# Kernel tuning notes

Measured on AMD Instinct MI355X. Metric: run time of the kernel, lower is better.

## Reference

```python
import jax, jax.numpy as jnp
import numpy as np

N_HEADS = 4
D_K = 64


def setup_inputs() -> dict:
    key = jax.random.key(0)
    k1, k2, k3, k4, k5 = jax.random.split(key, 5)
    C = 256
    return {
        "x": jax.random.normal(k1, (16, C, 32, 32), dtype=jnp.float32),
        "W_qkv": jax.random.normal(k2, (C, N_HEADS * D_K * 3), dtype=jnp.float32) * (C ** -0.5),
        "b_qkv": jax.random.normal(k3, (N_HEADS * D_K * 3,), dtype=jnp.float32) * 0.02,
        "W_out": jax.random.normal(k4, (N_HEADS * D_K, C), dtype=jnp.float32) * ((N_HEADS * D_K) ** -0.5),
        "b_out": jax.random.normal(k5, (C,), dtype=jnp.float32) * 0.02,
    }


def reference(x, W_qkv, b_qkv, W_out, b_out):
    # NOTE: the original forward never applies self.norm and ignores t.
    B, C, H, W = x.shape
    N = H * W
    scale = D_K ** -0.5
    xf = x.reshape(B, C, N).transpose(0, 2, 1)            # [B, N, C]
    qkv = (xf @ W_qkv + b_qkv).reshape(B, N, N_HEADS, 3 * D_K)
    q, k, v = jnp.split(qkv, 3, axis=-1)                  # each [B, N, H, dk]
    attn = jnp.einsum('bihd,bjhd->bijh', q, k) * scale    # [B, N, N, H]
    attn = jax.nn.softmax(attn, axis=2)                   # softmax over keys (j)
    res = jnp.einsum('bijh,bjhd->bihd', attn, v)          # [B, N, H, dk]
    res = res.reshape(B, N, N_HEADS * D_K)
    res = res @ W_out + b_out + xf                        # residual on flattened x
    return res.transpose(0, 2, 1).reshape(B, C, H, W)
```

## Files before the change

kernel.cpp:

```cpp
#include <hip/hip_runtime.h>
#include <math.h>

#define NN 1024

typedef __attribute__((ext_vector_type(8))) __bf16 bf16x8;
typedef __attribute__((ext_vector_type(4))) __bf16 bf16x4;
typedef __attribute__((ext_vector_type(4))) float f32x4;

__device__ __forceinline__ unsigned short f2bf(float f) {
    __bf16 h = (__bf16)f;
    return *(unsigned short*)&h;
}
__device__ __forceinline__ ushort4 pack4(float a, float b, float c, float d) {
    bf16x4 v;
    v[0] = (__bf16)a; v[1] = (__bf16)b; v[2] = (__bf16)c; v[3] = (__bf16)d;
    return *(ushort4*)&v;
}

__device__ __forceinline__ void async_cp16(const unsigned short* g, unsigned short* l) {
    __builtin_amdgcn_global_load_lds(
        (const __attribute__((address_space(1))) unsigned int*)g,
        (__attribute__((address_space(3))) unsigned int*)l,
        16, 0, 0);
}

__global__ __launch_bounds__(256) void prep_transpose(
    const float* __restrict__ x, const float* __restrict__ Wq,
    const float* __restrict__ Wo,
    unsigned short* __restrict__ xb, unsigned short* __restrict__ Wqt,
    unsigned short* __restrict__ Wot)
{
    __shared__ __align__(16) unsigned short T[64 * 72];
    const int bx = blockIdx.x;
    const int rt = blockIdx.y;
    const float* src; unsigned short* dst; int ncol, c0;
    if (bx < 256) {
        int b = bx >> 4; int ct = bx & 15;
        src = x + (size_t)b * 256 * 1024; dst = xb + (size_t)b * 1024 * 256;
        ncol = 1024; c0 = ct * 64;
    } else if (bx < 268) {
        src = Wq; dst = Wqt; ncol = 768; c0 = (bx - 256) * 64;
    } else {
        src = Wo; dst = Wot; ncol = 256; c0 = (bx - 268) * 64;
    }
    const int t = threadIdx.x;
    #pragma unroll
    for (int i = 0; i < 4; ++i) {
        int r  = i * 16 + (t >> 4);
        int c4 = (t & 15) * 4;
        float4 v = *(const float4*)&src[(size_t)(rt * 64 + r) * ncol + c0 + c4];
        *(ushort4*)&T[r * 72 + c4] = pack4(v.x, v.y, v.z, v.w);
    }
    __syncthreads();
    #pragma unroll
    for (int i = 0; i < 2; ++i) {
        int task = t + 256 * i;
        int c = task & 63, rs = task >> 6;
        ushort u8[8];
        #pragma unroll
        for (int k = 0; k < 8; ++k) u8[k] = T[(rs * 8 + k) * 72 + c];
        *(uint4*)&dst[(size_t)(c0 + c) * 256 + rt * 64 + rs * 8] = *(uint4*)u8;
    }
}

__global__ __launch_bounds__(256, 4) void qkv_gemm(
    const unsigned short* __restrict__ xb, const unsigned short* __restrict__ Wqt,
    const float* __restrict__ bias,
    unsigned short* __restrict__ Qb, unsigned short* __restrict__ Kb,
    unsigned short* __restrict__ Vtb)
{
    __shared__ __align__(16) unsigned short As[128 * 40];
    __shared__ __align__(16) unsigned short Bs[128 * 40];
    const int jt = blockIdx.x;
    const int m0 = blockIdx.y * 128;
    const int b  = m0 >> 10;
    const int n0 = m0 & 1023;
    const int t = threadIdx.x;
    const int w = t >> 6, lane = t & 63, quad = lane >> 4, cc = lane & 15;
    const int wm = (w & 1) * 64;
    const int wj = (w >> 1) * 64;

    f32x4 acc[4][4];
    #pragma unroll
    for (int ms = 0; ms < 4; ++ms)
        #pragma unroll
        for (int js = 0; js < 4; ++js) acc[ms][js] = (f32x4)(0.f);

    for (int k0 = 0; k0 < 256; k0 += 32) {
        __syncthreads();
        #pragma unroll
        for (int i = 0; i < 2; ++i) {
            int flat = t + 256 * i;
            int row = flat >> 2, seg = flat & 3;
            *(uint4*)&As[row * 40 + seg * 8] =
                *(const uint4*)&xb[(size_t)(m0 + row) * 256 + k0 + seg * 8];
            *(uint4*)&Bs[row * 40 + seg * 8] =
                *(const uint4*)&Wqt[(size_t)(jt * 128 + row) * 256 + k0 + seg * 8];
        }
        __syncthreads();
        bf16x8 af[4], bfr[4];
        #pragma unroll
        for (int ms = 0; ms < 4; ++ms)
            af[ms] = *(bf16x8*)&As[(wm + ms * 16 + cc) * 40 + quad * 8];
        #pragma unroll
        for (int js = 0; js < 4; ++js)
            bfr[js] = *(bf16x8*)&Bs[(wj + js * 16 + cc) * 40 + quad * 8];
        #pragma unroll
        for (int ms = 0; ms < 4; ++ms)
            #pragma unroll
            for (int js = 0; js < 4; ++js)
                acc[ms][js] = __builtin_amdgcn_mfma_f32_16x16x32_bf16(
                    af[ms], bfr[js], acc[ms][js], 0, 0, 0);
    }

    const int chunk = jt * 2 + (w >> 1);
    const int h = chunk / 3, type = chunk % 3;
    const size_t bh = (size_t)b * 4 + h;
    float bias_r[4];
    #pragma unroll
    for (int js = 0; js < 4; ++js) bias_r[js] = bias[jt * 128 + wj + js * 16 + cc];

    if (type == 2) {
        #pragma unroll
        for (int ms = 0; ms < 4; ++ms)
            #pragma unroll
            for (int js = 0; js < 4; ++js) {
                int dd = js * 16 + cc;
                int n = n0 + wm + ms * 16 + quad * 4;
                *(ushort4*)&Vtb[(bh * 64 + dd) * NN + n] =
                    pack4(acc[ms][js][0] + bias_r[js], acc[ms][js][1] + bias_r[js],
                          acc[ms][js][2] + bias_r[js], acc[ms][js][3] + bias_r[js]);
            }
    } else {
        unsigned short* dst = type ? Kb : Qb;
        const float sc = type ? 1.0f : 0.18033688011112042f;
        #pragma unroll
        for (int ms = 0; ms < 4; ++ms)
            #pragma unroll
            for (int js = 0; js < 4; ++js)
                #pragma unroll
                for (int r = 0; r < 4; ++r) {
                    int n = n0 + wm + ms * 16 + quad * 4 + r;
                    dst[(bh * NN + n) * 64 + js * 16 + cc] =
                        f2bf((acc[ms][js][r] + bias_r[js]) * sc);
                }
    }
}

__global__ __launch_bounds__(256, 4) void flash_attn(
    const unsigned short* __restrict__ Qb, const unsigned short* __restrict__ Kb,
    const unsigned short* __restrict__ Vtb, unsigned short* __restrict__ resb)
{
    __shared__ __align__(16) unsigned short QP[4096];
    __shared__ __align__(16) unsigned short Ks0[4096];
    __shared__ __align__(16) unsigned short Ks1[4096];
    __shared__ __align__(16) unsigned short Vt0[4096];
    __shared__ __align__(16) unsigned short Vt1[4096];

    const int blk = blockIdx.x;
    const int qt = blk & 15;
    const int h  = (blk >> 4) & 3;
    const int b  = blk >> 6;
    const int t  = threadIdx.x;
    const int w  = t >> 6;
    const int lane = t & 63;
    const int quad = lane >> 4;
    const int c    = lane & 15;

    const size_t bh = (size_t)(b * 4 + h);
    const unsigned short* Qg = Qb  + bh * NN * 64;
    const unsigned short* Kg = Kb  + bh * NN * 64;
    const unsigned short* Vg = Vtb + bh * 64 * NN;

    #pragma unroll
    for (int i = 0; i < 2; ++i) {
        int f = i * 256 + t;
        int row = f >> 3;
        int gc  = (f & 7) ^ (row & 7);
        async_cp16(&Qg[(size_t)(qt * 64 + row) * 64 + gc * 8], &QP[f * 8]);
        async_cp16(&Kg[(size_t)row * 64 + gc * 8], &Ks0[f * 8]);
        async_cp16(&Vg[(size_t)row * NN + gc * 8], &Vt0[f * 8]);
    }
    __syncthreads();

    bf16x8 qf[2];
    #pragma unroll
    for (int ks = 0; ks < 2; ++ks) {
        int sc_ = (ks * 4 + quad) ^ (c & 7);
        qf[ks] = *(bf16x8*)&QP[((w * 16 + c) * 8 + sc_) * 8];
    }

    float m_i = -INFINITY, l_i = 0.f;
    f32x4 O[4];
    #pragma unroll
    for (int dt = 0; dt < 4; ++dt) O[dt] = (f32x4)(0.f);

    auto step = [&](int kt, const unsigned short* curK, const unsigned short* curV,
                    unsigned short* nxtK, unsigned short* nxtV,
                    bool pref, bool bar) {
        if (bar) __syncthreads();
        if (pref) {
            int ktn = kt + 1;
            #pragma unroll
            for (int i = 0; i < 2; ++i) {
                int f = i * 256 + t;
                int row = f >> 3;
                int gc  = (f & 7) ^ (row & 7);
                async_cp16(&Kg[(size_t)(ktn * 64 + row) * 64 + gc * 8], &nxtK[f * 8]);
                async_cp16(&Vg[(size_t)row * NN + ktn * 64 + gc * 8], &nxtV[f * 8]);
            }
        }

        f32x4 S[4];
        #pragma unroll
        for (int jt = 0; jt < 4; ++jt) S[jt] = (f32x4)(0.f);
        #pragma unroll
        for (int ks = 0; ks < 2; ++ks) {
            #pragma unroll
            for (int jt = 0; jt < 4; ++jt) {
                int sc_ = (ks * 4 + quad) ^ (c & 7);
                bf16x8 kf = *(bf16x8*)&curK[((jt * 16 + c) * 8 + sc_) * 8];
                S[jt] = __builtin_amdgcn_mfma_f32_16x16x32_bf16(kf, qf[ks], S[jt], 0, 0, 0);
            }
        }

        float tj[4];
        #pragma unroll
        for (int jt = 0; jt < 4; ++jt)
            tj[jt] = fmaxf(fmaxf(S[jt][0], S[jt][1]), fmaxf(S[jt][2], S[jt][3]));
        float mt = fmaxf(fmaxf(tj[0], tj[1]), fmaxf(tj[2], tj[3]));
        mt = fmaxf(mt, __shfl_xor(mt, 16));
        mt = fmaxf(mt, __shfl_xor(mt, 32));
        float mn = fmaxf(m_i, mt);
        float alpha = __builtin_amdgcn_exp2f(m_i - mn);
        float p[4][4], rsj[4];
        #pragma unroll
        for (int jt = 0; jt < 4; ++jt) {
            #pragma unroll
            for (int r = 0; r < 4; ++r)
                p[jt][r] = __builtin_amdgcn_exp2f(S[jt][r] - mn);
            rsj[jt] = (p[jt][0] + p[jt][1]) + (p[jt][2] + p[jt][3]);
        }
        float rs = (rsj[0] + rsj[1]) + (rsj[2] + rsj[3]);
        rs += __shfl_xor(rs, 16);
        rs += __shfl_xor(rs, 32);
        l_i = l_i * alpha + rs;
        m_i = mn;

        #pragma unroll
        for (int jt = 0; jt < 4; ++jt) {
            int scw = (jt * 2 + (quad >> 1)) ^ (c & 7);
            *(ushort4*)&QP[(w * 16 + c) * 64 + scw * 8 + (quad & 1) * 4] =
                pack4(p[jt][0], p[jt][1], p[jt][2], p[jt][3]);
        }

        float alpha_r[4];
        #pragma unroll
        for (int r = 0; r < 4; ++r) alpha_r[r] = __shfl(alpha, quad * 4 + r);
        #pragma unroll
        for (int dt = 0; dt < 4; ++dt)
            #pragma unroll
            for (int r = 0; r < 4; ++r) O[dt][r] *= alpha_r[r];

        #pragma unroll
        for (int js = 0; js < 2; ++js) {
            int scp = (js * 4 + quad) ^ (c & 7);
            bf16x8 pf = *(bf16x8*)&QP[(w * 16 + c) * 64 + scp * 8];
            #pragma unroll
            for (int dt = 0; dt < 4; ++dt) {
                int sc_ = (js * 4 + quad) ^ (c & 7);
                bf16x8 vf = *(bf16x8*)&curV[((dt * 16 + c) * 8 + sc_) * 8];
                O[dt] = __builtin_amdgcn_mfma_f32_16x16x32_bf16(pf, vf, O[dt], 0, 0, 0);
            }
        }
    };

    step(0, Ks0, Vt0, Ks1, Vt1, true, false);
    for (int kt2 = 0; kt2 < 7; ++kt2) {
        int kt = 2 * kt2 + 1;
        step(kt,     Ks1, Vt1, Ks0, Vt0, true, true);
        step(kt + 1, Ks0, Vt0, Ks1, Vt1, true, true);
    }
    step(15, Ks1, Vt1, Ks0, Vt0, false, true);

    float linv[4];
    #pragma unroll
    for (int r = 0; r < 4; ++r) linv[r] = 1.f / __shfl(l_i, quad * 4 + r);
    #pragma unroll
    for (int dt = 0; dt < 4; ++dt)
        #pragma unroll
        for (int r = 0; r < 4; ++r) {
            int row = qt * 64 + w * 16 + quad * 4 + r;
            resb[((size_t)(b * NN + row)) * 256 + h * 64 + dt * 16 + c] =
                f2bf(O[dt][r] * linv[r]);
        }
}

__global__ __launch_bounds__(256, 4) void out_gemm(
    const unsigned short* __restrict__ resb, const unsigned short* __restrict__ Wot,
    const float* __restrict__ bias, const float* __restrict__ x,
    float* __restrict__ out)
{
    __shared__ __align__(16) unsigned short As[64 * 40];
    __shared__ __align__(16) unsigned short Bs[64 * 40];
    const int n0 = blockIdx.x * 64;
    const int c0 = blockIdx.y * 64;
    const int b  = blockIdx.z;
    const int t = threadIdx.x;
    const int w = t >> 6, lane = t & 63, quad = lane >> 4, cc = lane & 15;
    const int wm = (w & 1) * 32;
    const int wj = (w >> 1) * 32;

    f32x4 acc[2][2];
    #pragma unroll
    for (int ms = 0; ms < 2; ++ms)
        #pragma unroll
        for (int js = 0; js < 2; ++js) acc[ms][js] = (f32x4)(0.f);

    for (int k0 = 0; k0 < 256; k0 += 32) {
        __syncthreads();
        {
            int r = t >> 2, seg = t & 3;
            *(uint4*)&As[r * 40 + seg * 8] =
                *(const uint4*)&resb[((size_t)b * NN + n0 + r) * 256 + k0 + seg * 8];
            *(uint4*)&Bs[r * 40 + seg * 8] =
                *(const uint4*)&Wot[(size_t)(c0 + r) * 256 + k0 + seg * 8];
        }
        __syncthreads();
        bf16x8 af[2], bfr[2];
        #pragma unroll
        for (int ms = 0; ms < 2; ++ms)
            af[ms] = *(bf16x8*)&As[(wm + ms * 16 + cc) * 40 + quad * 8];
        #pragma unroll
        for (int js = 0; js < 2; ++js)
            bfr[js] = *(bf16x8*)&Bs[(wj + js * 16 + cc) * 40 + quad * 8];
        #pragma unroll
        for (int ms = 0; ms < 2; ++ms)
            #pragma unroll
            for (int js = 0; js < 2; ++js)
                acc[ms][js] = __builtin_amdgcn_mfma_f32_16x16x32_bf16(
                    af[ms], bfr[js], acc[ms][js], 0, 0, 0);
    }

    #pragma unroll
    for (int js = 0; js < 2; ++js) {
        int cI = c0 + wj + js * 16 + cc;
        float bi = bias[cI];
        #pragma unroll
        for (int ms = 0; ms < 2; ++ms) {
            int n = n0 + wm + ms * 16 + quad * 4;
            size_t off = ((size_t)b * 256 + cI) * NN + n;
            float4 xr = *(const float4*)&x[off];
            float4 o;
            o.x = acc[ms][js][0] + bi + xr.x;
            o.y = acc[ms][js][1] + bi + xr.y;
            o.z = acc[ms][js][2] + bi + xr.z;
            o.w = acc[ms][js][3] + bi + xr.w;
            *(float4*)&out[off] = o;
        }
    }
}

extern "C" void kernel_launch(void* const* d_in, const int* in_sizes, int n_in,
                              void* d_out, int out_size, void* d_ws, size_t ws_size,
                              hipStream_t stream)
{
    const float* x     = (const float*)d_in[0];
    const float* W_qkv = (const float*)d_in[1];
    const float* b_qkv = (const float*)d_in[2];
    const float* W_out = (const float*)d_in[3];
    const float* b_out = (const float*)d_in[4];
    float* out = (float*)d_out;

    char* wsc = (char*)d_ws;
    unsigned short* xb   = (unsigned short*)(wsc);
    unsigned short* Wqt  = (unsigned short*)(wsc + ((size_t)8 << 20));
    unsigned short* Wot  = (unsigned short*)(wsc + ((size_t)8 << 20) + ((size_t)512 << 10));
    unsigned short* Qb   = (unsigned short*)(wsc + ((size_t)9  << 20));
    unsigned short* Kb   = (unsigned short*)(wsc + ((size_t)17 << 20));
    unsigned short* Vtb  = (unsigned short*)(wsc + ((size_t)25 << 20));
    unsigned short* resb = (unsigned short*)(wsc + ((size_t)33 << 20));

    prep_transpose<<<dim3(272, 4), 256, 0, stream>>>(x, W_qkv, W_out, xb, Wqt, Wot);
    qkv_gemm<<<dim3(6, 128), 256, 0, stream>>>(xb, Wqt, b_qkv, Qb, Kb, Vtb);
    flash_attn<<<dim3(1024), 256, 0, stream>>>(Qb, Kb, Vtb, resb);
    out_gemm<<<dim3(16, 4, 16), 256, 0, stream>>>(resb, Wot, b_out, x, out);
}
```

Measured before the change: 138.0 us.

## Give each flash-attention wave two query sub-tiles to reuse K/V fragments

Each flash_attn block now runs 2 waves (128 threads) instead of 4, and each wave handles 32 query rows as two 16-row sub-tiles. Each K and V fragment read from LDS feeds two MFMAs, halving LDS reads per unit of MFMA work, and the async loads are spread over the fewer threads. In exchange there are fewer waves per block to hide latency, register pressure rises, and launch bounds drop to 2 blocks per CU, which may lower occupancy.

```diff
diff --git a/kernel.cpp b/kernel.cpp
--- a/kernel.cpp
+++ b/kernel.cpp
@@ -147,7 +147,7 @@
     }
 }
 
-__global__ __launch_bounds__(256, 4) void flash_attn(
+__global__ __launch_bounds__(128, 2) void flash_attn(
     const unsigned short* __restrict__ Qb, const unsigned short* __restrict__ Kb,
     const unsigned short* __restrict__ Vtb, unsigned short* __restrict__ resb)
 {
@@ -173,8 +173,8 @@
     const unsigned short* Vg = Vtb + bh * 64 * NN;
 
     #pragma unroll
-    for (int i = 0; i < 2; ++i) {
-        int f = i * 256 + t;
+    for (int i = 0; i < 4; ++i) {
+        int f = i * 128 + t;
         int row = f >> 3;
         int gc  = (f & 7) ^ (row & 7);
         async_cp16(&Qg[(size_t)(qt * 64 + row) * 64 + gc * 8], &QP[f * 8]);
@@ -183,17 +183,21 @@
     }
     __syncthreads();
 
-    bf16x8 qf[2];
-    #pragma unroll
-    for (int ks = 0; ks < 2; ++ks) {
-        int sc_ = (ks * 4 + quad) ^ (c & 7);
-        qf[ks] = *(bf16x8*)&QP[((w * 16 + c) * 8 + sc_) * 8];
-    }
-
-    float m_i = -INFINITY, l_i = 0.f;
-    f32x4 O[4];
-    #pragma unroll
-    for (int dt = 0; dt < 4; ++dt) O[dt] = (f32x4)(0.f);
+    bf16x8 qf[2][2];
+    #pragma unroll
+    for (int u = 0; u < 2; ++u)
+        #pragma unroll
+        for (int ks = 0; ks < 2; ++ks) {
+            int sc_ = (ks * 4 + quad) ^ (c & 7);
+            qf[u][ks] = *(bf16x8*)&QP[((w * 32 + u * 16 + c) * 8 + sc_) * 8];
+        }
+
+    float m_i[2] = {-INFINITY, -INFINITY}, l_i[2] = {0.f, 0.f};
+    f32x4 O[2][4];
+    #pragma unroll
+    for (int u = 0; u < 2; ++u)
+        #pragma unroll
+        for (int dt = 0; dt < 4; ++dt) O[u][dt] = (f32x4)(0.f);
 
     auto step = [&](int kt, const unsigned short* curK, const unsigned short* curV,
                     unsigned short* nxtK, unsigned short* nxtV,
@@ -202,8 +206,8 @@
         if (pref) {
             int ktn = kt + 1;
             #pragma unroll
-            for (int i = 0; i < 2; ++i) {
-                int f = i * 256 + t;
+            for (int i = 0; i < 4; ++i) {
+                int f = i * 128 + t;
                 int row = f >> 3;
                 int gc  = (f & 7) ^ (row & 7);
                 async_cp16(&Kg[(size_t)(ktn * 64 + row) * 64 + gc * 8], &nxtK[f * 8]);
@@ -211,66 +215,87 @@
             }
         }
 
-        f32x4 S[4];
-        #pragma unroll
-        for (int jt = 0; jt < 4; ++jt) S[jt] = (f32x4)(0.f);
+        f32x4 S[2][4];
+        #pragma unroll
+        for (int u = 0; u < 2; ++u)
+            #pragma unroll
+            for (int jt = 0; jt < 4; ++jt) S[u][jt] = (f32x4)(0.f);
         #pragma unroll
         for (int ks = 0; ks < 2; ++ks) {
             #pragma unroll
             for (int jt = 0; jt < 4; ++jt) {
                 int sc_ = (ks * 4 + quad) ^ (c & 7);
                 bf16x8 kf = *(bf16x8*)&curK[((jt * 16 + c) * 8 + sc_) * 8];
-                S[jt] = __builtin_amdgcn_mfma_f32_16x16x32_bf16(kf, qf[ks], S[jt], 0, 0, 0);
-            }
-        }
-
-        float tj[4];
-        #pragma unroll
-        for (int jt = 0; jt < 4; ++jt)
-            tj[jt] = fmaxf(fmaxf(S[jt][0], S[jt][1]), fmaxf(S[jt][2], S[jt][3]));
-        float mt = fmaxf(fmaxf(tj[0], tj[1]), fmaxf(tj[2], tj[3]));
-        mt = fmaxf(mt, __shfl_xor(mt, 16));
-        mt = fmaxf(mt, __shfl_xor(mt, 32));
-        float mn = fmaxf(m_i, mt);
-        float alpha = __builtin_amdgcn_exp2f(m_i - mn);
-        float p[4][4], rsj[4];
-        #pragma unroll
-        for (int jt = 0; jt < 4; ++jt) {
-            #pragma unroll
-            for (int r = 0; r < 4; ++r)
-                p[jt][r] = __builtin_amdgcn_exp2f(S[jt][r] - mn);
-            rsj[jt] = (p[jt][0] + p[jt][1]) + (p[jt][2] + p[jt][3]);
-        }
-        float rs = (rsj[0] + rsj[1]) + (rsj[2] + rsj[3]);
-        rs += __shfl_xor(rs, 16);
-        rs += __shfl_xor(rs, 32);
-        l_i = l_i * alpha + rs;
-        m_i = mn;
-
-        #pragma unroll
-        for (int jt = 0; jt < 4; ++jt) {
-            int scw = (jt * 2 + (quad >> 1)) ^ (c & 7);
-            *(ushort4*)&QP[(w * 16 + c) * 64 + scw * 8 + (quad & 1) * 4] =
-                pack4(p[jt][0], p[jt][1], p[jt][2], p[jt][3]);
-        }
-
-        float alpha_r[4];
-        #pragma unroll
-        for (int r = 0; r < 4; ++r) alpha_r[r] = __shfl(alpha, quad * 4 + r);
-        #pragma unroll
-        for (int dt = 0; dt < 4; ++dt)
-            #pragma unroll
-            for (int r = 0; r < 4; ++r) O[dt][r] *= alpha_r[r];
+                #pragma unroll
+                for (int u = 0; u < 2; ++u)
+                    S[u][jt] = __builtin_amdgcn_mfma_f32_16x16x32_bf16(
+                        kf, qf[u][ks], S[u][jt], 0, 0, 0);
+            }
+        }
+
+        float p[2][4][4], alpha[2];
+        #pragma unroll
+        for (int u = 0; u < 2; ++u) {
+            float tj[4];
+            #pragma unroll
+            for (int jt = 0; jt < 4; ++jt)
+                tj[jt] = fmaxf(fmaxf(S[u][jt][0], S[u][jt][1]),
+                               fmaxf(S[u][jt][2], S[u][jt][3]));
+            float mt = fmaxf(fmaxf(tj[0], tj[1]), fmaxf(tj[2], tj[3]));
+            mt = fmaxf(mt, __shfl_xor(mt, 16));
+            mt = fmaxf(mt, __shfl_xor(mt, 32));
+            float mn = fmaxf(m_i[u], mt);
+            alpha[u] = __builtin_amdgcn_exp2f(m_i[u] - mn);
+            float rsj[4];
+            #pragma unroll
+            for (int jt = 0; jt < 4; ++jt) {
+                #pragma unroll
+                for (int r = 0; r < 4; ++r)
+                    p[u][jt][r] = __builtin_amdgcn_exp2f(S[u][jt][r] - mn);
+                rsj[jt] = (p[u][jt][0] + p[u][jt][1]) + (p[u][jt][2] + p[u][jt][3]);
+            }
+            float rs = (rsj[0] + rsj[1]) + (rsj[2] + rsj[3]);
+            rs += __shfl_xor(rs, 16);
+            rs += __shfl_xor(rs, 32);
+            l_i[u] = l_i[u] * alpha[u] + rs;
+            m_i[u] = mn;
+        }
+
+        #pragma unroll
+        for (int u = 0; u < 2; ++u)
+            #pragma unroll
+            for (int jt = 0; jt < 4; ++jt) {
+                int scw = (jt * 2 + (quad >> 1)) ^ (c & 7);
+                *(ushort4*)&QP[(w * 32 + u * 16 + c) * 64 + scw * 8 + (quad & 1) * 4] =
+                    pack4(p[u][jt][0], p[u][jt][1], p[u][jt][2], p[u][jt][3]);
+            }
+
+        #pragma unroll
+        for (int u = 0; u < 2; ++u) {
+            float alpha_r[4];
+            #pragma unroll
+            for (int r = 0; r < 4; ++r) alpha_r[r] = __shfl(alpha[u], quad * 4 + r);
+            #pragma unroll
+            for (int dt = 0; dt < 4; ++dt)
+                #pragma unroll
+                for (int r = 0; r < 4; ++r) O[u][dt][r] *= alpha_r[r];
+        }
 
         #pragma unroll
         for (int js = 0; js < 2; ++js) {
             int scp = (js * 4 + quad) ^ (c & 7);
-            bf16x8 pf = *(bf16x8*)&QP[(w * 16 + c) * 64 + scp * 8];
+            bf16x8 pf[2];
+            #pragma unroll
+            for (int u = 0; u < 2; ++u)
+                pf[u] = *(bf16x8*)&QP[(w * 32 + u * 16 + c) * 64 + scp * 8];
             #pragma unroll
             for (int dt = 0; dt < 4; ++dt) {
                 int sc_ = (js * 4 + quad) ^ (c & 7);
                 bf16x8 vf = *(bf16x8*)&curV[((dt * 16 + c) * 8 + sc_) * 8];
-                O[dt] = __builtin_amdgcn_mfma_f32_16x16x32_bf16(pf, vf, O[dt], 0, 0, 0);
+                #pragma unroll
+                for (int u = 0; u < 2; ++u)
+                    O[u][dt] = __builtin_amdgcn_mfma_f32_16x16x32_bf16(
+                        pf[u], vf, O[u][dt], 0, 0, 0);
             }
         }
     };
@@ -283,17 +308,20 @@
     }
     step(15, Ks1, Vt1, Ks0, Vt0, false, true);
 
-    float linv[4];
-    #pragma unroll
-    for (int r = 0; r < 4; ++r) linv[r] = 1.f / __shfl(l_i, quad * 4 + r);
-    #pragma unroll
-    for (int dt = 0; dt < 4; ++dt)
-        #pragma unroll
-        for (int r = 0; r < 4; ++r) {
-            int row = qt * 64 + w * 16 + quad * 4 + r;
-            resb[((size_t)(b * NN + row)) * 256 + h * 64 + dt * 16 + c] =
-                f2bf(O[dt][r] * linv[r]);
-        }
+    #pragma unroll
+    for (int u = 0; u < 2; ++u) {
+        float linv[4];
+        #pragma unroll
+        for (int r = 0; r < 4; ++r) linv[r] = 1.f / __shfl(l_i[u], quad * 4 + r);
+        #pragma unroll
+        for (int dt = 0; dt < 4; ++dt)
+            #pragma unroll
+            for (int r = 0; r < 4; ++r) {
+                int row = qt * 64 + w * 32 + u * 16 + quad * 4 + r;
+                resb[((size_t)(b * NN + row)) * 256 + h * 64 + dt * 16 + c] =
+                    f2bf(O[u][dt][r] * linv[r]);
+            }
+    }
 }
 
 __global__ __launch_bounds__(256, 4) void out_gemm(
@@ -383,6 +411,6 @@
 
     prep_transpose<<<dim3(272, 4), 256, 0, stream>>>(x, W_qkv, W_out, xb, Wqt, Wot);
     qkv_gemm<<<dim3(6, 128), 256, 0, stream>>>(xb, Wqt, b_qkv, Qb, Kb, Vtb);
-    flash_attn<<<dim3(1024), 256, 0, stream>>>(Qb, Kb, Vtb, resb);
+    flash_attn<<<dim3(1024), 128, 0, stream>>>(Qb, Kb, Vtb, resb);
     out_gemm<<<dim3(16, 4, 16), 256, 0, stream>>>(resb, Wot, b_out, x, out);
 }
```

Result: no change. 139.1 us (+0.8%).
